# Kernel tuning notes

Hardware: AMD Instinct MI355X
Metric: run time of the kernel (lower is better)

Reference implementation:

```python
import jax, jax.numpy as jnp
import numpy as np

D_MODEL = 1024
N_HEADS = 16
HEAD_DIM = D_MODEL // N_HEADS
N_EXPERTS = 8
TOP_K = 2
D_FF = 4096
B, T = 4, 1024
EPS = 1e-5


def setup_inputs() -> dict:
    key = jax.random.key(0)
    ks = jax.random.split(key, 12)
    s = lambda fan_in: 1.0 / np.sqrt(fan_in)
    x = jax.random.normal(ks[0], (B, T, D_MODEL), dtype=jnp.float32)
    # additive causal mask (0 on/below diagonal, -inf above)
    mask = jnp.where(jnp.tril(jnp.ones((T, T), dtype=bool)), 0.0, -1e9).astype(jnp.float32)
    return {
        "x": x,
        "mask": mask,
        "ln1_g": jnp.ones((D_MODEL,), jnp.float32),
        "ln1_b": jnp.zeros((D_MODEL,), jnp.float32),
        "w_qkv": jax.random.normal(ks[1], (D_MODEL, 3 * D_MODEL), jnp.float32) * s(D_MODEL),
        "w_proj": jax.random.normal(ks[2], (D_MODEL, D_MODEL), jnp.float32) * s(D_MODEL),
        "b_proj": jnp.zeros((D_MODEL,), jnp.float32),
        "ln2_g": jnp.ones((D_MODEL,), jnp.float32),
        "ln2_b": jnp.zeros((D_MODEL,), jnp.float32),
        "w_router": jax.random.normal(ks[3], (D_MODEL, N_EXPERTS), jnp.float32) * s(D_MODEL),
        "w1": jax.random.normal(ks[4], (N_EXPERTS, D_MODEL, D_FF), jnp.float32) * s(D_MODEL),
        "b1": jnp.zeros((N_EXPERTS, D_FF), jnp.float32),
        "w2": jax.random.normal(ks[5], (N_EXPERTS, D_FF, D_MODEL), jnp.float32) * s(D_FF),
        "b2": jnp.zeros((N_EXPERTS, D_MODEL), jnp.float32),
    }


def _layer_norm(x, g, b):
    mu = jnp.mean(x, axis=-1, keepdims=True)
    var = jnp.var(x, axis=-1, keepdims=True)
    return (x - mu) * jax.lax.rsqrt(var + EPS) * g + b


def _rope(q, k):
    # q, k: [B, H, T, hd]; GPT-NeoX half-split rotary
    t = q.shape[2]
    half = HEAD_DIM // 2
    inv_freq = 1.0 / (10000.0 ** (jnp.arange(0, half, dtype=jnp.float32) / half))
    ang = jnp.arange(t, dtype=jnp.float32)[:, None] * inv_freq[None, :]  # [T, half]
    cos = jnp.concatenate([jnp.cos(ang), jnp.cos(ang)], axis=-1)[None, None]  # [1,1,T,hd]
    sin = jnp.concatenate([jnp.sin(ang), jnp.sin(ang)], axis=-1)[None, None]

    def rot_half(u):
        u1, u2 = jnp.split(u, 2, axis=-1)
        return jnp.concatenate([-u2, u1], axis=-1)

    return q * cos + rot_half(q) * sin, k * cos + rot_half(k) * sin


def _attention(x, mask, w_qkv, w_proj, b_proj):
    b, t, _ = x.shape
    qkv = x @ w_qkv  # [B,T,3D]
    q, k, v = jnp.split(qkv, 3, axis=-1)
    rs = lambda u: u.reshape(b, t, N_HEADS, HEAD_DIM).transpose(0, 2, 1, 3)
    q, k, v = rs(q), rs(k), rs(v)
    q, k = _rope(q, k)
    scale = HEAD_DIM ** -0.5
    scores = jnp.einsum("bhqd,bhkd->bhqk", q, k) * scale + mask
    attn = jax.nn.softmax(scores, axis=-1)
    out = jnp.einsum("bhqk,bhkd->bhqd", attn, v)
    out = out.transpose(0, 2, 1, 3).reshape(b, t, D_MODEL)
    return out @ w_proj + b_proj


def _moe(x, w_router, w1, b1, w2, b2):
    b, t, d = x.shape
    xf = x.reshape(-1, d)  # [N, d]
    logits = xf @ w_router  # [N, E]
    probs = jax.nn.softmax(logits, axis=-1)
    top_v, top_i = jax.lax.top_k(probs, TOP_K)  # [N, k]
    weights = top_v / jnp.sum(top_v, axis=-1, keepdims=True)
    onehot = jax.nn.one_hot(top_i, N_EXPERTS, dtype=xf.dtype)  # [N, k, E]
    gates = jnp.einsum("nk,nke->ne", weights, onehot)  # [N, E]
    # dense grouped-FFN over experts
    h = jax.nn.gelu(jnp.einsum("nd,edf->enf", xf, w1) + b1[:, None, :], approximate=False)
    y = jnp.einsum("enf,efd->end", h, w2) + b2[:, None, :]
    out = jnp.einsum("end,ne->nd", y, gates).reshape(b, t, d)
    # load-balancing aux loss (Switch-style)
    dispatch = jnp.sum(onehot, axis=1)  # [N, E]
    frac = jnp.mean(dispatch, axis=0) / TOP_K
    mean_prob = jnp.mean(probs, axis=0)
    aux = N_EXPERTS * jnp.sum(frac * mean_prob)
    return out, aux


def reference(x, mask, ln1_g, ln1_b, w_qkv, w_proj, b_proj, ln2_g, ln2_b,
              w_router, w1, b1, w2, b2):
    # dropout is identity (eval / p=0)
    x = x + _attention(_layer_norm(x, ln1_g, ln1_b), mask, w_qkv, w_proj, b_proj)
    moe_out, aux = _moe(_layer_norm(x, ln2_g, ln2_b), w_router, w1, b1, w2, b2)
    x = x + moe_out
    return x, aux
```

## Files before the change

### kernel.cpp

```cpp
#include <hip/hip_runtime.h>
#include <math.h>


typedef __bf16 bf16;
typedef __bf16 bf16x8 __attribute__((ext_vector_type(8)));
typedef float  f32x4  __attribute__((ext_vector_type(4)));

#define D_MODEL 1024
#define SEQ     1024
#define NTOK    4096
#define DFF     4096
#define NEXP    8

__device__ __forceinline__ f32x4 mfma16(bf16x8 a, bf16x8 b, f32x4 c) {
  return __builtin_amdgcn_mfma_f32_16x16x32_bf16(a, b, c, 0, 0, 0);
}

__device__ __forceinline__ void async_cp16(void* lds, const void* g) {
  __builtin_amdgcn_global_load_lds(
      (__attribute__((address_space(1))) void*)(void*)g,
      (__attribute__((address_space(3))) void*)lds, 16, 0, 0);
}

__device__ __forceinline__ int swz(int row, int col) {
  return row * 64 + (col ^ (((row ^ (row >> 3)) & 7) << 3));
}

template<bool SPLIT>
__device__ __forceinline__ void gemm_core(
    const bf16* __restrict__ Ahi, const bf16* __restrict__ Alo,
    const bf16* __restrict__ Bhi, const bf16* __restrict__ Blo,
    long aOff0, long aOff1, long bOff0, long bOff1,
    int K, bf16* As, bf16* Bs, f32x4 acc[4][4])
{
  const int tid  = threadIdx.x;
  const int lane = tid & 63, w = tid >> 6;
  const int fr   = lane & 15, quad = lane >> 4;
  const int wm   = w >> 1,    wn   = w & 1;
  bf16* AsD0 = As + (w * 16) * 32;
  bf16* AsD1 = As + (64 + w * 16) * 32;
  bf16* BsD0 = Bs + (w * 16) * 32;
  bf16* BsD1 = Bs + (64 + w * 16) * 32;
  const int nph = SPLIT ? 3 : 1;
  for (int ph = 0; ph < nph; ++ph) {
    const bf16* Ap = (ph == 1) ? Alo : Ahi;
    const bf16* Bp = (ph == 2) ? Blo : Bhi;
    for (int k0 = 0; k0 < K; k0 += 32) {
      async_cp16(AsD0, Ap + aOff0 + k0);
      async_cp16(AsD1, Ap + aOff1 + k0);
      async_cp16(BsD0, Bp + bOff0 + k0);
      async_cp16(BsD1, Bp + bOff1 + k0);
      __syncthreads();
      bf16x8 af[4], bfv[4];
#pragma unroll
      for (int mi = 0; mi < 4; ++mi)
        af[mi] = *(const bf16x8*)&As[(wm * 64 + mi * 16 + fr) * 32 + quad * 8];
#pragma unroll
      for (int ni = 0; ni < 4; ++ni)
        bfv[ni] = *(const bf16x8*)&Bs[(wn * 64 + ni * 16 + fr) * 32 + quad * 8];
#pragma unroll
      for (int mi = 0; mi < 4; ++mi)
#pragma unroll
        for (int ni = 0; ni < 4; ++ni)
          acc[mi][ni] = mfma16(af[mi], bfv[ni], acc[mi][ni]);
      __syncthreads();
    }
  }
}

__global__ void k_transpose_cast(const float* __restrict__ in,
                                 bf16* __restrict__ oh, bf16* __restrict__ ol,
                                 int K, int N)
{
  const long zo = (long)blockIdx.z * K * N;
  __shared__ float tile[32][33];
  const int tx = threadIdx.x & 31, ty = threadIdx.x >> 5;
  const int r0 = blockIdx.y * 32, c0 = blockIdx.x * 32;
#pragma unroll
  for (int j = 0; j < 4; ++j)
    tile[ty + 8 * j][tx] = in[zo + (long)(r0 + ty + 8 * j) * N + (c0 + tx)];
  __syncthreads();
#pragma unroll
  for (int j = 0; j < 4; ++j) {
    float v = tile[tx][ty + 8 * j];
    long  o = zo + (long)(c0 + ty + 8 * j) * K + (r0 + tx);
    bf16 hh = (bf16)v;
    oh[o] = hh;
    if (ol) ol[o] = (bf16)(v - (float)hh);
  }
}

__global__ __launch_bounds__(256) void k_layernorm(
    const float* __restrict__ x, const float* __restrict__ g,
    const float* __restrict__ b, bf16* __restrict__ oh, bf16* __restrict__ ol)
{
  const int tok = blockIdx.x, tid = threadIdx.x;
  const float4 v = ((const float4*)(x + (long)tok * D_MODEL))[tid];
  float s  = v.x + v.y + v.z + v.w;
  float s2 = v.x * v.x + v.y * v.y + v.z * v.z + v.w * v.w;
#pragma unroll
  for (int off = 1; off < 64; off <<= 1) {
    s  += __shfl_xor(s, off);
    s2 += __shfl_xor(s2, off);
  }
  __shared__ float red[8];
  if ((tid & 63) == 0) { red[tid >> 6] = s; red[4 + (tid >> 6)] = s2; }
  __syncthreads();
  s  = red[0] + red[1] + red[2] + red[3];
  s2 = red[4] + red[5] + red[6] + red[7];
  const float mu   = s * (1.0f / D_MODEL);
  const float var  = s2 * (1.0f / D_MODEL) - mu * mu;
  const float rstd = 1.0f / sqrtf(var + 1e-5f);
  const float4 gg = ((const float4*)g)[tid];
  const float4 bb = ((const float4*)b)[tid];
  float o0 = (v.x - mu) * rstd * gg.x + bb.x;
  float o1 = (v.y - mu) * rstd * gg.y + bb.y;
  float o2 = (v.z - mu) * rstd * gg.z + bb.z;
  float o3 = (v.w - mu) * rstd * gg.w + bb.w;
  const long base = (long)tok * D_MODEL + tid * 4;
  bf16 h0 = (bf16)o0, h1 = (bf16)o1, h2 = (bf16)o2, h3 = (bf16)o3;
  oh[base + 0] = h0; oh[base + 1] = h1; oh[base + 2] = h2; oh[base + 3] = h3;
  if (ol) {
    ol[base + 0] = (bf16)(o0 - (float)h0);
    ol[base + 1] = (bf16)(o1 - (float)h1);
    ol[base + 2] = (bf16)(o2 - (float)h2);
    ol[base + 3] = (bf16)(o3 - (float)h3);
  }
}

__global__ __launch_bounds__(256, 2) void k_gemm_qkv(
    const bf16* __restrict__ Ah, const bf16* __restrict__ Al,
    const bf16* __restrict__ Bh, const bf16* __restrict__ Bl,
    float* __restrict__ out)
{
  __shared__ __align__(16) bf16 As[128 * 32];
  __shared__ __align__(16) bf16 Bs[128 * 32];
  const int tid = threadIdx.x, lane = tid & 63, w = tid >> 6;
  const int fr = lane & 15, quad = lane >> 4;
  const int wm = w >> 1, wn = w & 1;
  const int m0 = blockIdx.y * 128, n0 = blockIdx.x * 128;
  const int lrow = w * 16 + (lane >> 2), colk = (lane & 3) * 8;
  long aOff0 = (long)(m0 + lrow) * D_MODEL + colk;
  long aOff1 = aOff0 + 64L * D_MODEL;
  long bOff0 = (long)(n0 + lrow) * D_MODEL + colk;
  long bOff1 = bOff0 + 64L * D_MODEL;
  f32x4 acc[4][4];
  f32x4 zv = {0.f, 0.f, 0.f, 0.f};
#pragma unroll
  for (int i = 0; i < 4; ++i)
#pragma unroll
    for (int j = 0; j < 4; ++j) acc[i][j] = zv;
  gemm_core<true>(Ah, Al, Bh, Bl, aOff0, aOff1, bOff0, bOff1, D_MODEL, As, Bs, acc);
#pragma unroll
  for (int mi = 0; mi < 4; ++mi)
#pragma unroll
    for (int ni = 0; ni < 4; ++ni) {
      const int col = n0 + wn * 64 + ni * 16 + fr;
#pragma unroll
      for (int r = 0; r < 4; ++r) {
        const int row = m0 + wm * 64 + mi * 16 + quad * 4 + r;
        out[(long)row * 3072 + col] = acc[mi][ni][r];
      }
    }
}

__global__ __launch_bounds__(256) void k_rope(
    const float* __restrict__ qkv,
    bf16* __restrict__ qh, bf16* __restrict__ ql,
    bf16* __restrict__ kh, bf16* __restrict__ kl,
    bf16* __restrict__ vh, bf16* __restrict__ vl)
{
  const int tok = blockIdx.x;
  const int t = tok & (SEQ - 1), bb = tok >> 10;
  const int tid = threadIdx.x;
  const float ft = (float)t;
  for (int it = tid; it < 512; it += 256) {
    const int hh = it >> 5, i = it & 31;
    const float inv = powf(10000.0f, -(float)i * (1.0f / 32.0f));
    const float ang = ft * inv;
    float sn, cs;
    sincosf(ang, &sn, &cs);
    const long src = (long)tok * 3072 + hh * 64 + i;
    const float q0 = qkv[src], q1 = qkv[src + 32];
    const float k0 = qkv[src + 1024], k1 = qkv[src + 1024 + 32];
    const float qo0 = q0 * cs - q1 * sn, qo1 = q1 * cs + q0 * sn;
    const float ko0 = k0 * cs - k1 * sn, ko1 = k1 * cs + k0 * sn;
    const long dst = ((long)(bb * 16 + hh) * SEQ + t) * 64 + i;
    bf16 x;
    x = (bf16)qo0; qh[dst] = x;      ql[dst] = (bf16)(qo0 - (float)x);
    x = (bf16)qo1; qh[dst + 32] = x; ql[dst + 32] = (bf16)(qo1 - (float)x);
    x = (bf16)ko0; kh[dst] = x;      kl[dst] = (bf16)(ko0 - (float)x);
    x = (bf16)ko1; kh[dst + 32] = x; kl[dst + 32] = (bf16)(ko1 - (float)x);
  }
  for (int it = tid; it < 1024; it += 256) {
    const int hh = it >> 6, d = it & 63;
    const float vv = qkv[(long)tok * 3072 + 2048 + it];
    const long dst = ((long)(bb * 16 + hh) * SEQ + t) * 64 + d;
    bf16 x = (bf16)vv;
    vh[dst] = x; vl[dst] = (bf16)(vv - (float)x);
  }
}

__global__ __launch_bounds__(256, 3) void k_flash(
    const bf16* __restrict__ qh, const bf16* __restrict__ ql,
    const bf16* __restrict__ kh, const bf16* __restrict__ kl,
    const bf16* __restrict__ vh, const bf16* __restrict__ vl,
    bf16* __restrict__ oh, bf16* __restrict__ ol)
{
  const int qt = blockIdx.x, bhid = blockIdx.y;
  const int tid = threadIdx.x, lane = tid & 63, w = tid >> 6;
  const int fr = lane & 15, quad = lane >> 4;
  __shared__ __align__(16) bf16 QP0[64 * 64];
  __shared__ __align__(16) bf16 QP1[64 * 64];
  __shared__ __align__(16) bf16 Kh[64 * 64], Kl[64 * 64];
  __shared__ __align__(16) bf16 Vh[64 * 64], Vl[64 * 64];

  const long qbase = ((long)bhid * SEQ + qt * 64) * 64;
  for (int c = tid; c < 512; c += 256) {
    const int row = c >> 3, c8 = (c & 7) << 3;
    *(uint4*)&QP0[swz(row, c8)] = *(const uint4*)&qh[qbase + row * 64 + c8];
    *(uint4*)&QP1[swz(row, c8)] = *(const uint4*)&ql[qbase + row * 64 + c8];
  }
  __syncthreads();
  bf16x8 aQh[2], aQl[2];
#pragma unroll
  for (int kk = 0; kk < 2; ++kk) {
    aQh[kk] = *(const bf16x8*)&QP0[swz(w * 16 + fr, kk * 32 + quad * 8)];
    aQl[kk] = *(const bf16x8*)&QP1[swz(w * 16 + fr, kk * 32 + quad * 8)];
  }
  f32x4 o[4];
  f32x4 zv = {0.f, 0.f, 0.f, 0.f};
#pragma unroll
  for (int ct = 0; ct < 4; ++ct) o[ct] = zv;
  float m_r[4], l_r[4];
#pragma unroll
  for (int r = 0; r < 4; ++r) { m_r[r] = -1e30f; l_r[r] = 0.f; }

  for (int kt = 0; kt <= qt; ++kt) {
    __syncthreads();
    const long kbase = ((long)bhid * SEQ + kt * 64) * 64;
    for (int c = tid; c < 512; c += 256) {
      const int row = c >> 3, c8 = (c & 7) << 3;
      *(uint4*)&Kh[swz(row, c8)] = *(const uint4*)&kh[kbase + row * 64 + c8];
      *(uint4*)&Kl[swz(row, c8)] = *(const uint4*)&kl[kbase + row * 64 + c8];
      uint4 uh = *(const uint4*)&vh[kbase + row * 64 + c8];
      uint4 ul = *(const uint4*)&vl[kbase + row * 64 + c8];
      const bf16* vph = (const bf16*)&uh;
      const bf16* vpl = (const bf16*)&ul;
#pragma unroll
      for (int j = 0; j < 8; ++j) {
        Vh[swz(c8 + j, row)] = vph[j];
        Vl[swz(c8 + j, row)] = vpl[j];
      }
    }
    __syncthreads();

    f32x4 s[4];
#pragma unroll
    for (int nt = 0; nt < 4; ++nt) s[nt] = zv;
#pragma unroll
    for (int nt = 0; nt < 4; ++nt)
#pragma unroll
      for (int kk = 0; kk < 2; ++kk) {
        bf16x8 bh8 = *(const bf16x8*)&Kh[swz(nt * 16 + fr, kk * 32 + quad * 8)];
        bf16x8 bl8 = *(const bf16x8*)&Kl[swz(nt * 16 + fr, kk * 32 + quad * 8)];
        s[nt] = mfma16(aQh[kk], bh8, s[nt]);
        s[nt] = mfma16(aQl[kk], bh8, s[nt]);
        s[nt] = mfma16(aQh[kk], bl8, s[nt]);
      }
    const int qloc = w * 16 + quad * 4;
#pragma unroll
    for (int nt = 0; nt < 4; ++nt)
#pragma unroll
      for (int r = 0; r < 4; ++r) {
        float sv = s[nt][r] * 0.125f;
        if (kt == qt && (nt * 16 + fr) > (qloc + r)) sv = -1e30f;
        s[nt][r] = sv;
      }
    float al4[4];
#pragma unroll
    for (int r = 0; r < 4; ++r) {
      float m = fmaxf(fmaxf(s[0][r], s[1][r]), fmaxf(s[2][r], s[3][r]));
#pragma unroll
      for (int off = 1; off < 16; off <<= 1) m = fmaxf(m, __shfl_xor(m, off));
      const float mn = fmaxf(m_r[r], m);
      al4[r] = expf(m_r[r] - mn);
      m_r[r] = mn;
    }
    float pmat[4][4], ls4[4];
#pragma unroll
    for (int r = 0; r < 4; ++r) ls4[r] = 0.f;
#pragma unroll
    for (int nt = 0; nt < 4; ++nt)
#pragma unroll
      for (int r = 0; r < 4; ++r) {
        const float p = expf(s[nt][r] - m_r[r]);
        pmat[nt][r] = p;
        ls4[r] += p;
      }
#pragma unroll
    for (int r = 0; r < 4; ++r) {
      float l = ls4[r];
#pragma unroll
      for (int off = 1; off < 16; off <<= 1) l += __shfl_xor(l, off);
      l_r[r] = l_r[r] * al4[r] + l;
      o[0][r] *= al4[r]; o[1][r] *= al4[r]; o[2][r] *= al4[r]; o[3][r] *= al4[r];
    }
    bf16* Pw0 = QP0 + w * 1024;
    bf16* Pw1 = QP1 + w * 1024;
#pragma unroll
    for (int nt = 0; nt < 4; ++nt)
#pragma unroll
      for (int r = 0; r < 4; ++r) {
        const float p = pmat[nt][r];
        bf16 hh2 = (bf16)p;
        Pw0[swz(quad * 4 + r, nt * 16 + fr)] = hh2;
        Pw1[swz(quad * 4 + r, nt * 16 + fr)] = (bf16)(p - (float)hh2);
      }
    __syncthreads();
#pragma unroll
    for (int kk = 0; kk < 2; ++kk) {
      bf16x8 aPh = *(const bf16x8*)&Pw0[swz(fr, kk * 32 + quad * 8)];
      bf16x8 aPl = *(const bf16x8*)&Pw1[swz(fr, kk * 32 + quad * 8)];
#pragma unroll
      for (int ct = 0; ct < 4; ++ct) {
        bf16x8 bVh = *(const bf16x8*)&Vh[swz(ct * 16 + fr, kk * 32 + quad * 8)];
        bf16x8 bVl = *(const bf16x8*)&Vl[swz(ct * 16 + fr, kk * 32 + quad * 8)];
        o[ct] = mfma16(aPh, bVh, o[ct]);
        o[ct] = mfma16(aPl, bVh, o[ct]);
        o[ct] = mfma16(aPh, bVl, o[ct]);
      }
    }
  }
  const int b_ = bhid >> 4, h_ = bhid & 15;
#pragma unroll
  for (int ct = 0; ct < 4; ++ct)
#pragma unroll
    for (int r = 0; r < 4; ++r) {
      const int tokn = b_ * SEQ + qt * 64 + w * 16 + quad * 4 + r;
      const int col = h_ * 64 + ct * 16 + fr;
      const float val = o[ct][r] / l_r[r];
      bf16 hh3 = (bf16)val;
      oh[(long)tokn * D_MODEL + col] = hh3;
      ol[(long)tokn * D_MODEL + col] = (bf16)(val - (float)hh3);
    }
}

__global__ __launch_bounds__(256, 2) void k_gemm_proj(
    const bf16* __restrict__ Ah, const bf16* __restrict__ Al,
    const bf16* __restrict__ Bh, const bf16* __restrict__ Bl,
    const float* __restrict__ bproj, const float* __restrict__ xin,
    float* __restrict__ out)
{
  __shared__ __align__(16) bf16 As[128 * 32];
  __shared__ __align__(16) bf16 Bs[128 * 32];
  const int tid = threadIdx.x, lane = tid & 63, w = tid >> 6;
  const int fr = lane & 15, quad = lane >> 4;
  const int wm = w >> 1, wn = w & 1;
  const int m0 = blockIdx.y * 128, n0 = blockIdx.x * 128;
  const int lrow = w * 16 + (lane >> 2), colk = (lane & 3) * 8;
  long aOff0 = (long)(m0 + lrow) * D_MODEL + colk;
  long aOff1 = aOff0 + 64L * D_MODEL;
  long bOff0 = (long)(n0 + lrow) * D_MODEL + colk;
  long bOff1 = bOff0 + 64L * D_MODEL;
  f32x4 acc[4][4];
  f32x4 zv = {0.f, 0.f, 0.f, 0.f};
#pragma unroll
  for (int i = 0; i < 4; ++i)
#pragma unroll
    for (int j = 0; j < 4; ++j) acc[i][j] = zv;
  gemm_core<true>(Ah, Al, Bh, Bl, aOff0, aOff1, bOff0, bOff1, D_MODEL, As, Bs, acc);
#pragma unroll
  for (int mi = 0; mi < 4; ++mi)
#pragma unroll
    for (int ni = 0; ni < 4; ++ni) {
      const int col = n0 + wn * 64 + ni * 16 + fr;
#pragma unroll
      for (int r = 0; r < 4; ++r) {
        const int row = m0 + wm * 64 + mi * 16 + quad * 4 + r;
        out[(long)row * D_MODEL + col] =
            acc[mi][ni][r] + bproj[col] + xin[(long)row * D_MODEL + col];
      }
    }
}

__global__ __launch_bounds__(256) void k_router(
    const float* __restrict__ x1, const float* __restrict__ g,
    const float* __restrict__ b, const float* __restrict__ wr,
    int2* __restrict__ topi, float2* __restrict__ topg,
    float* __restrict__ pbuf)
{
  const int tok = blockIdx.x, tid = threadIdx.x;
  const float4 v = ((const float4*)(x1 + (long)tok * D_MODEL))[tid];
  float s  = v.x + v.y + v.z + v.w;
  float s2 = v.x * v.x + v.y * v.y + v.z * v.z + v.w * v.w;
#pragma unroll
  for (int off = 1; off < 64; off <<= 1) {
    s  += __shfl_xor(s, off);
    s2 += __shfl_xor(s2, off);
  }
  __shared__ float red[8];
  __shared__ float lr[4][8];
  if ((tid & 63) == 0) { red[tid >> 6] = s; red[4 + (tid >> 6)] = s2; }
  __syncthreads();
  s  = red[0] + red[1] + red[2] + red[3];
  s2 = red[4] + red[5] + red[6] + red[7];
  const float mu   = s * (1.0f / D_MODEL);
  const float var  = s2 * (1.0f / D_MODEL) - mu * mu;
  const float rstd = 1.0f / sqrtf(var + 1e-5f);
  const float4 gg = ((const float4*)g)[tid];
  const float4 bb = ((const float4*)b)[tid];
  float n4[4];
  n4[0] = (v.x - mu) * rstd * gg.x + bb.x;
  n4[1] = (v.y - mu) * rstd * gg.y + bb.y;
  n4[2] = (v.z - mu) * rstd * gg.z + bb.z;
  n4[3] = (v.w - mu) * rstd * gg.w + bb.w;
  float part[8];
#pragma unroll
  for (int e = 0; e < 8; ++e) part[e] = 0.f;
  const float* wrow = wr + (long)tid * 4 * 8;
#pragma unroll
  for (int c = 0; c < 4; ++c)
#pragma unroll
    for (int e = 0; e < 8; ++e) part[e] += n4[c] * wrow[c * 8 + e];
#pragma unroll
  for (int off = 1; off < 64; off <<= 1)
#pragma unroll
    for (int e = 0; e < 8; ++e) part[e] += __shfl_xor(part[e], off);
  if ((tid & 63) == 0)
#pragma unroll
    for (int e = 0; e < 8; ++e) lr[tid >> 6][e] = part[e];
  __syncthreads();
  if (tid == 0) {
    float lg[8];
#pragma unroll
    for (int e = 0; e < 8; ++e) lg[e] = lr[0][e] + lr[1][e] + lr[2][e] + lr[3][e];
    float mx = lg[0];
#pragma unroll
    for (int e = 1; e < 8; ++e) mx = fmaxf(mx, lg[e]);
    float pe[8], ssum = 0.f;
#pragma unroll
    for (int e = 0; e < 8; ++e) { pe[e] = expf(lg[e] - mx); ssum += pe[e]; }
    const float inv = 1.0f / ssum;
    int i1 = -1, i2 = -1;
    float v1 = -1.f, v2 = -1.f;
#pragma unroll
    for (int e = 0; e < 8; ++e) {
      const float p = pe[e] * inv;
      pbuf[(long)tok * 8 + e] = p;
      if (p > v1)      { v2 = v1; i2 = i1; v1 = p; i1 = e; }
      else if (p > v2) { v2 = p; i2 = e; }
    }
    const float wsum = v1 + v2;
    topi[tok] = make_int2(i1, i2);
    topg[tok] = make_float2(v1 / wsum, v2 / wsum);
  }
}

__global__ __launch_bounds__(256) void k_scatter(
    const int2* __restrict__ topi, const float2* __restrict__ topg,
    int* __restrict__ ecnt, int* __restrict__ perm, float* __restrict__ gatew)
{
  __shared__ int hcnt[NEXP];
  __shared__ int hbase[NEXP];
  const int tid = threadIdx.x;
  const int tok = blockIdx.x * 256 + tid;
  if (tid < NEXP) hcnt[tid] = 0;
  __syncthreads();
  const int2 ti = topi[tok];
  const float2 tg = topg[tok];
  const int r1 = atomicAdd(&hcnt[ti.x], 1);
  const int r2 = atomicAdd(&hcnt[ti.y], 1);
  __syncthreads();
  if (tid < NEXP) hbase[tid] = atomicAdd(&ecnt[tid], hcnt[tid]);
  __syncthreads();
  const int p1 = hbase[ti.x] + r1;
  perm[ti.x * NTOK + p1] = tok; gatew[ti.x * NTOK + p1] = tg.x;
  const int p2 = hbase[ti.y] + r2;
  perm[ti.y * NTOK + p2] = tok; gatew[ti.y * NTOK + p2] = tg.y;
}

__global__ __launch_bounds__(256) void k_finalize(
    const int* __restrict__ ecnt, const float* __restrict__ pbuf,
    int* __restrict__ eoff, float* __restrict__ aux_out)
{
  __shared__ float partial[256];
  const int tid = threadIdx.x;
  const int e = tid & 7, i0 = tid >> 3;
  float sum = 0.f;
  for (int i = i0; i < NTOK; i += 32) sum += pbuf[(long)i * 8 + e];
  partial[tid] = sum;
  __syncthreads();
  if (tid < 8) {
    float ps = 0.f;
#pragma unroll
    for (int j = 0; j < 32; ++j) ps += partial[j * 8 + tid];
    partial[tid] = ps;
  }
  __syncthreads();
  if (tid == 0) {
    int off = 0;
    float aux = 0.f;
    for (int e2 = 0; e2 < 8; ++e2) {
      eoff[e2] = off;
      off += (ecnt[e2] + 127) & ~127;
      aux += ((float)ecnt[e2] * (1.0f / (NTOK * 2.0f))) * (partial[e2] * (1.0f / NTOK));
    }
    aux_out[0] = 8.0f * aux;
  }
}

__global__ __launch_bounds__(256, 2) void k_gemm_ffn1(
    const bf16* __restrict__ A, const bf16* __restrict__ w1t,
    const float* __restrict__ b1, const int* __restrict__ ecnt,
    const int* __restrict__ eoff, const int* __restrict__ perm,
    bf16* __restrict__ h)
{
  const int e = blockIdx.y >> 5, mt = blockIdx.y & 31;
  const int cnt = ecnt[e];
  if (mt * 128 >= cnt) return;
  __shared__ __align__(16) bf16 As[128 * 32];
  __shared__ __align__(16) bf16 Bs[128 * 32];
  const int tid = threadIdx.x, lane = tid & 63, w = tid >> 6;
  const int fr = lane & 15, quad = lane >> 4;
  const int wm = w >> 1, wn = w & 1;
  const int n0 = blockIdx.x * 128;
  const int lrow = w * 16 + (lane >> 2), colk = (lane & 3) * 8;
  int i0 = mt * 128 + lrow;
  int i1 = i0 + 64;
  i0 = min(i0, cnt - 1);
  i1 = min(i1, cnt - 1);
  const int* pe = perm + e * NTOK;
  long aOff0 = (long)pe[i0] * D_MODEL + colk;
  long aOff1 = (long)pe[i1] * D_MODEL + colk;
  const bf16* B = w1t + (long)e * DFF * D_MODEL;
  long bOff0 = (long)(n0 + lrow) * D_MODEL + colk;
  long bOff1 = bOff0 + 64L * D_MODEL;
  f32x4 acc[4][4];
  f32x4 zv = {0.f, 0.f, 0.f, 0.f};
#pragma unroll
  for (int i = 0; i < 4; ++i)
#pragma unroll
    for (int j = 0; j < 4; ++j) acc[i][j] = zv;
  gemm_core<false>(A, A, B, B, aOff0, aOff1, bOff0, bOff1, D_MODEL, As, Bs, acc);
  const int hbase = eoff[e] + mt * 128;
#pragma unroll
  for (int mi = 0; mi < 4; ++mi)
#pragma unroll
    for (int ni = 0; ni < 4; ++ni) {
      const int col = n0 + wn * 64 + ni * 16 + fr;
#pragma unroll
      for (int r = 0; r < 4; ++r) {
        const int irow = wm * 64 + mi * 16 + quad * 4 + r;
        const float vv = acc[mi][ni][r] + b1[e * DFF + col];
        const float ge = 0.5f * vv * (1.0f + erff(vv * 0.70710678118654752f));
        h[(long)(hbase + irow) * DFF + col] = (bf16)ge;
      }
    }
}

__global__ __launch_bounds__(256, 2) void k_gemm_ffn2(
    const bf16* __restrict__ hbuf, const bf16* __restrict__ w2t,
    const float* __restrict__ b2, const int* __restrict__ ecnt,
    const int* __restrict__ eoff, const int* __restrict__ perm,
    const float* __restrict__ gatew, float* __restrict__ out)
{
  const int e = blockIdx.y >> 5, mt = blockIdx.y & 31;
  const int cnt = ecnt[e];
  if (mt * 128 >= cnt) return;
  __shared__ __align__(16) bf16 As[128 * 32];
  __shared__ __align__(16) bf16 Bs[128 * 32];
  const int tid = threadIdx.x, lane = tid & 63, w = tid >> 6;
  const int fr = lane & 15, quad = lane >> 4;
  const int wm = w >> 1, wn = w & 1;
  const int n0 = blockIdx.x * 128;
  const int lrow = w * 16 + (lane >> 2), colk = (lane & 3) * 8;
  const bf16* A = hbuf + (long)(eoff[e] + mt * 128) * DFF;
  long aOff0 = (long)lrow * DFF + colk;
  long aOff1 = aOff0 + 64L * DFF;
  const bf16* B = w2t + (long)e * D_MODEL * DFF;
  long bOff0 = (long)(n0 + lrow) * DFF + colk;
  long bOff1 = bOff0 + 64L * DFF;
  f32x4 acc[4][4];
  f32x4 zv = {0.f, 0.f, 0.f, 0.f};
#pragma unroll
  for (int i = 0; i < 4; ++i)
#pragma unroll
    for (int j = 0; j < 4; ++j) acc[i][j] = zv;
  gemm_core<false>(A, A, B, B, aOff0, aOff1, bOff0, bOff1, DFF, As, Bs, acc);
#pragma unroll
  for (int mi = 0; mi < 4; ++mi)
#pragma unroll
    for (int ni = 0; ni < 4; ++ni) {
      const int col = n0 + wn * 64 + ni * 16 + fr;
#pragma unroll
      for (int r = 0; r < 4; ++r) {
        const int irow = wm * 64 + mi * 16 + quad * 4 + r;
        const int gi = mt * 128 + irow;
        if (gi < cnt) {
          const int tok = perm[e * NTOK + gi];
          const float gw = gatew[e * NTOK + gi];
          const float vv = acc[mi][ni][r] + b2[e * D_MODEL + col];
          atomicAdd(&out[(long)tok * D_MODEL + col], vv * gw);
        }
      }
    }
}

extern "C" void kernel_launch(void* const* d_in, const int* in_sizes, int n_in,
                              void* d_out, int out_size, void* d_ws, size_t ws_size,
                              hipStream_t stream) {
  const float* x     = (const float*)d_in[0];
  const float* ln1g  = (const float*)d_in[2];
  const float* ln1b  = (const float*)d_in[3];
  const float* wqkv  = (const float*)d_in[4];
  const float* wproj = (const float*)d_in[5];
  const float* bproj = (const float*)d_in[6];
  const float* ln2g  = (const float*)d_in[7];
  const float* ln2b  = (const float*)d_in[8];
  const float* wrout = (const float*)d_in[9];
  const float* w1    = (const float*)d_in[10];
  const float* b1    = (const float*)d_in[11];
  const float* w2    = (const float*)d_in[12];
  const float* b2    = (const float*)d_in[13];
  float* out = (float*)d_out;

  char* p = (char*)d_ws;
  auto alloc = [&](size_t n) { char* r = p; p += (n + 255) & ~(size_t)255; return r; };

  bf16* wqkvT_h = (bf16*)alloc(3072L * 1024 * 2);
  bf16* wqkvT_l = (bf16*)alloc(3072L * 1024 * 2);
  bf16* wprojT_h = (bf16*)alloc(1024L * 1024 * 2);
  bf16* wprojT_l = (bf16*)alloc(1024L * 1024 * 2);
  bf16* w1T = (bf16*)alloc(8L * 4096 * 1024 * 2);
  bf16* w2T = (bf16*)alloc(8L * 1024 * 4096 * 2);
  bf16* ln_h = (bf16*)alloc(4096L * 1024 * 2);
  bf16* ln_l = (bf16*)alloc(4096L * 1024 * 2);
  bf16* attn_h = (bf16*)alloc(4096L * 1024 * 2);
  bf16* attn_l = (bf16*)alloc(4096L * 1024 * 2);
  int*   perm  = (int*)alloc(8L * 4096 * 4);
  float* gatew = (float*)alloc(8L * 4096 * 4);
  int2*  topi  = (int2*)alloc(4096L * 8);
  float2* topg = (float2*)alloc(4096L * 8);
  float* pbuf  = (float*)alloc(4096L * 8 * 4);
  char*  ctrl  = alloc(256);
  int*   ecnt  = (int*)ctrl;
  int*   eoff  = (int*)(ctrl + 64);
  char* big = alloc(100663296);
  float* qkvf = (float*)big;
  bf16* qh = (bf16*)(big + 50331648);
  bf16* ql = qh + 4194304;
  bf16* kh = ql + 4194304;
  bf16* kl = kh + 4194304;
  bf16* vh = kl + 4194304;
  bf16* vl = vh + 4194304;
  bf16* hbuf = (bf16*)big;

  dim3 blk(256);

  k_transpose_cast<<<dim3(3072 / 32, 1024 / 32, 1), blk, 0, stream>>>(wqkv, wqkvT_h, wqkvT_l, 1024, 3072);
  k_transpose_cast<<<dim3(1024 / 32, 1024 / 32, 1), blk, 0, stream>>>(wproj, wprojT_h, wprojT_l, 1024, 1024);
  k_transpose_cast<<<dim3(4096 / 32, 1024 / 32, 8), blk, 0, stream>>>(w1, w1T, nullptr, 1024, 4096);
  k_transpose_cast<<<dim3(1024 / 32, 4096 / 32, 8), blk, 0, stream>>>(w2, w2T, nullptr, 4096, 1024);
  hipMemsetAsync(ctrl, 0, 256, stream);

  k_layernorm<<<4096, blk, 0, stream>>>(x, ln1g, ln1b, ln_h, ln_l);
  k_gemm_qkv<<<dim3(24, 32), blk, 0, stream>>>(ln_h, ln_l, wqkvT_h, wqkvT_l, qkvf);
  k_rope<<<4096, blk, 0, stream>>>(qkvf, qh, ql, kh, kl, vh, vl);
  k_flash<<<dim3(16, 64), blk, 0, stream>>>(qh, ql, kh, kl, vh, vl, attn_h, attn_l);
  k_gemm_proj<<<dim3(8, 32), blk, 0, stream>>>(attn_h, attn_l, wprojT_h, wprojT_l, bproj, x, out);

  k_layernorm<<<4096, blk, 0, stream>>>(out, ln2g, ln2b, ln_h, nullptr);
  k_router<<<4096, blk, 0, stream>>>(out, ln2g, ln2b, wrout, topi, topg, pbuf);
  k_scatter<<<16, blk, 0, stream>>>(topi, topg, ecnt, perm, gatew);
  k_finalize<<<1, blk, 0, stream>>>(ecnt, pbuf, eoff, out + 4194304);
  k_gemm_ffn1<<<dim3(32, 256), blk, 0, stream>>>(ln_h, w1T, b1, ecnt, eoff, perm, hbuf);
  k_gemm_ffn2<<<dim3(8, 256), blk, 0, stream>>>(hbuf, w2T, b2, ecnt, eoff, perm, gatew, out);
}
```

Before: 1.079 ms.

## Replace FFN2 scattered atomic adds with dense expert output buffer and combine kernel

The second expert GEMM now writes bias-added results densely into a per-expert-row fp32 buffer instead of doing gate-weighted atomicAdds into the scattered token rows. A new combine kernel reads each token's two expert rows, using positions recorded by the scatter kernel, and adds the gated sum into the output with vectorized loads. This removes roughly 8M global float atomics with poor locality. In exchange it adds a ~36MB intermediate write and read and one extra launch, and rows past cnt within padded tiles are written unconditionally into the buffer.

After: 1.058 ms. 2.0% less time.

```diff
diff --git a/kernel.cpp b/kernel.cpp
--- a/kernel.cpp
+++ b/kernel.cpp
@@ -458,8 +458,8 @@
 }
 
 __global__ __launch_bounds__(256) void k_scatter(
-    const int2* __restrict__ topi, const float2* __restrict__ topg,
-    int* __restrict__ ecnt, int* __restrict__ perm, float* __restrict__ gatew)
+    const int2* __restrict__ topi,
+    int* __restrict__ ecnt, int* __restrict__ perm, int2* __restrict__ pos)
 {
   __shared__ int hcnt[NEXP];
   __shared__ int hbase[NEXP];
@@ -468,16 +468,16 @@
   if (tid < NEXP) hcnt[tid] = 0;
   __syncthreads();
   const int2 ti = topi[tok];
-  const float2 tg = topg[tok];
   const int r1 = atomicAdd(&hcnt[ti.x], 1);
   const int r2 = atomicAdd(&hcnt[ti.y], 1);
   __syncthreads();
   if (tid < NEXP) hbase[tid] = atomicAdd(&ecnt[tid], hcnt[tid]);
   __syncthreads();
   const int p1 = hbase[ti.x] + r1;
-  perm[ti.x * NTOK + p1] = tok; gatew[ti.x * NTOK + p1] = tg.x;
+  perm[ti.x * NTOK + p1] = tok;
   const int p2 = hbase[ti.y] + r2;
-  perm[ti.y * NTOK + p2] = tok; gatew[ti.y * NTOK + p2] = tg.y;
+  perm[ti.y * NTOK + p2] = tok;
+  pos[tok] = make_int2(p1, p2);
 }
 
 __global__ __launch_bounds__(256) void k_finalize(
@@ -562,8 +562,7 @@
 __global__ __launch_bounds__(256, 2) void k_gemm_ffn2(
     const bf16* __restrict__ hbuf, const bf16* __restrict__ w2t,
     const float* __restrict__ b2, const int* __restrict__ ecnt,
-    const int* __restrict__ eoff, const int* __restrict__ perm,
-    const float* __restrict__ gatew, float* __restrict__ out)
+    const int* __restrict__ eoff, float* __restrict__ ybuf)
 {
   const int e = blockIdx.y >> 5, mt = blockIdx.y & 31;
   const int cnt = ecnt[e];
@@ -575,7 +574,8 @@
   const int wm = w >> 1, wn = w & 1;
   const int n0 = blockIdx.x * 128;
   const int lrow = w * 16 + (lane >> 2), colk = (lane & 3) * 8;
-  const bf16* A = hbuf + (long)(eoff[e] + mt * 128) * DFF;
+  const int rbase = eoff[e] + mt * 128;
+  const bf16* A = hbuf + (long)rbase * DFF;
   long aOff0 = (long)lrow * DFF + colk;
   long aOff1 = aOff0 + 64L * DFF;
   const bf16* B = w2t + (long)e * D_MODEL * DFF;
@@ -593,18 +593,35 @@
 #pragma unroll
     for (int ni = 0; ni < 4; ++ni) {
       const int col = n0 + wn * 64 + ni * 16 + fr;
+      const float bias = b2[e * D_MODEL + col];
 #pragma unroll
       for (int r = 0; r < 4; ++r) {
         const int irow = wm * 64 + mi * 16 + quad * 4 + r;
-        const int gi = mt * 128 + irow;
-        if (gi < cnt) {
-          const int tok = perm[e * NTOK + gi];
-          const float gw = gatew[e * NTOK + gi];
-          const float vv = acc[mi][ni][r] + b2[e * D_MODEL + col];
-          atomicAdd(&out[(long)tok * D_MODEL + col], vv * gw);
-        }
-      }
-    }
+        ybuf[(long)(rbase + irow) * D_MODEL + col] = acc[mi][ni][r] + bias;
+      }
+    }
+}
+
+__global__ __launch_bounds__(256) void k_combine(
+    const int2* __restrict__ topi, const float2* __restrict__ topg,
+    const int2* __restrict__ pos, const int* __restrict__ eoff,
+    const float* __restrict__ ybuf, float* __restrict__ out)
+{
+  const int tok = blockIdx.x, tid = threadIdx.x;
+  const int2 ti = topi[tok];
+  const int2 pp = pos[tok];
+  const float2 tg = topg[tok];
+  const long r1 = (long)eoff[ti.x] + pp.x;
+  const long r2 = (long)eoff[ti.y] + pp.y;
+  const float4 y1 = ((const float4*)(ybuf + r1 * D_MODEL))[tid];
+  const float4 y2 = ((const float4*)(ybuf + r2 * D_MODEL))[tid];
+  float4* po = (float4*)(out + (long)tok * D_MODEL) + tid;
+  float4 o = *po;
+  o.x += tg.x * y1.x + tg.y * y2.x;
+  o.y += tg.x * y1.y + tg.y * y2.y;
+  o.z += tg.x * y1.z + tg.y * y2.z;
+  o.w += tg.x * y1.w + tg.y * y2.w;
+  *po = o;
 }
 
 extern "C" void kernel_launch(void* const* d_in, const int* in_sizes, int n_in,
@@ -639,13 +656,14 @@
   bf16* attn_h = (bf16*)alloc(4096L * 1024 * 2);
   bf16* attn_l = (bf16*)alloc(4096L * 1024 * 2);
   int*   perm  = (int*)alloc(8L * 4096 * 4);
-  float* gatew = (float*)alloc(8L * 4096 * 4);
   int2*  topi  = (int2*)alloc(4096L * 8);
   float2* topg = (float2*)alloc(4096L * 8);
+  int2*  pos   = (int2*)alloc(4096L * 8);
   float* pbuf  = (float*)alloc(4096L * 8 * 4);
   char*  ctrl  = alloc(256);
   int*   ecnt  = (int*)ctrl;
   int*   eoff  = (int*)(ctrl + 64);
+  float* ybuf  = (float*)alloc(9216L * 1024 * 4);
   char* big = alloc(100663296);
   float* qkvf = (float*)big;
   bf16* qh = (bf16*)(big + 50331648);
@@ -672,8 +690,9 @@
 
   k_layernorm<<<4096, blk, 0, stream>>>(out, ln2g, ln2b, ln_h, nullptr);
   k_router<<<4096, blk, 0, stream>>>(out, ln2g, ln2b, wrout, topi, topg, pbuf);
-  k_scatter<<<16, blk, 0, stream>>>(topi, topg, ecnt, perm, gatew);
+  k_scatter<<<16, blk, 0, stream>>>(topi, ecnt, perm, pos);
   k_finalize<<<1, blk, 0, stream>>>(ecnt, pbuf, eoff, out + 4194304);
   k_gemm_ffn1<<<dim3(32, 256), blk, 0, stream>>>(ln_h, w1T, b1, ecnt, eoff, perm, hbuf);
-  k_gemm_ffn2<<<dim3(8, 256), blk, 0, stream>>>(hbuf, w2T, b2, ecnt, eoff, perm, gatew, out);
-}
+  k_gemm_ffn2<<<dim3(8, 256), blk, 0, stream>>>(hbuf, w2T, b2, ecnt, eoff, ybuf);
+  k_combine<<<4096, blk, 0, stream>>>(topi, topg, pos, eoff, ybuf, out);
+}
```
